# Kernel optimization log

Hardware: AMD Instinct MI355X
Metric: run time of the kernel (lower is better)

Reference implementation:

```python
import jax, jax.numpy as jnp
import numpy as np

C_HID = 128   # c = int(c2 * e) = 128
N_EXP = 4
TOP_K = 2


def conv2d(x, w, b, padding='SAME'):
    # x: [B,Cin,H,W], w: [Cout,Cin,kh,kw]
    out = jax.lax.conv_general_dilated(
        x, w, window_strides=(1, 1), padding=padding,
        dimension_numbers=('NCHW', 'OIHW', 'NCHW'))
    return out + b[None, :, None, None]


def silu(x):
    return x * jax.nn.sigmoid(x)


def setup_inputs() -> dict:
    key = jax.random.key(0)
    ks = jax.random.split(key, 10)
    B, C1, H, W = 16, 256, 80, 80
    c = C_HID
    s = 0.05
    return {
        'x': jax.random.normal(ks[0], (B, C1, H, W), jnp.float32),
        'W_cv1': jax.random.normal(ks[1], (2 * c, C1, 1, 1), jnp.float32) * s,
        'b_cv1': jax.random.normal(ks[2], (2 * c,), jnp.float32) * s,
        'W_r': jax.random.normal(ks[3], (N_EXP, c), jnp.float32) * s,
        'b_r': jax.random.normal(ks[4], (N_EXP,), jnp.float32) * s,
        'W_exp': jax.random.normal(ks[5], (N_EXP, c, c, 3, 3), jnp.float32) * s,
        'b_exp': jax.random.normal(ks[6], (N_EXP, c), jnp.float32) * s,
        'W_cv2': jax.random.normal(ks[7], (256, 3 * c, 1, 1), jnp.float32) * s,
        'b_cv2': jax.random.normal(ks[8], (256,), jnp.float32) * s,
    }


def reference(x, W_cv1, b_cv1, W_r, b_r, W_exp, b_exp, W_cv2, b_cv2):
    c = C_HID
    B = x.shape[0]
    # cv1: 1x1 conv -> SiLU (BN folded into bias), split into two branches
    y = silu(conv2d(x, W_cv1, b_cv1))           # [B, 2c, H, W]
    a, m = y[:, :c], y[:, c:]                   # each [B, c, H, W]

    # CrossModalRouter: GAP -> linear -> softmax -> top-k -> renormalize
    pooled = m.mean(axis=(2, 3))                # [B, c]
    logits = pooled @ W_r.T + b_r               # [B, E]
    probs = jax.nn.softmax(logits, axis=-1)
    w, idx = jax.lax.top_k(probs, TOP_K)        # [B, k]
    w = w / w.sum(axis=-1, keepdims=True)

    # dense sparse-gate: zeros except the top-k entries
    gate = jnp.zeros((B, N_EXP), x.dtype).at[jnp.arange(B)[:, None], idx].set(w)

    # DualModalExpertContainer: E independent 3x3 conv+SiLU experts, gated sum
    exp_out = jax.vmap(lambda we, be: silu(conv2d(m, we, be)))(W_exp, b_exp)  # [E,B,c,H,W]
    moe = jnp.einsum('be,ebchw->bchw', gate, exp_out)  # [B, c, H, W]

    # cv2 over concat([y0, y1, expert_out])
    out = silu(conv2d(jnp.concatenate([a, m, moe], axis=1), W_cv2, b_cv2))
    return out
```

## Files before the change

### kernel.cpp

```cpp
#include <hip/hip_runtime.h>
#include <hip/hip_bf16.h>

#define NPIX 6400
#define IMW 80
#define IMH 80

typedef __attribute__((ext_vector_type(8))) short short8;
typedef __attribute__((ext_vector_type(4))) float floatx4;

__device__ __forceinline__ float silu_f(float v) {
    return v / (1.0f + __expf(-v));
}
__device__ __forceinline__ unsigned short f2bf(float v) {
    __hip_bfloat16 h = __float2bfloat16(v);
    return *(unsigned short*)&h;
}


__global__ __launch_bounds__(256) void prep_swz1(
    const float* __restrict__ W1, __hip_bfloat16* __restrict__ Wt1s)
{
    int t = blockIdx.x * 256 + threadIdx.x;
    int mt = t >> 9, rem = t & 511;
    int ks = rem >> 6, lane = rem & 63;
    int col = lane & 15, quad = lane >> 4;
    const float* src = W1 + (size_t)(mt * 16 + col) * 256 + ks * 32 + quad * 8;
    unsigned short pk[8];
    #pragma unroll
    for (int j = 0; j < 8; ++j) pk[j] = f2bf(src[j]);
    *(uint4*)(Wt1s + (size_t)t * 8) = *(uint4*)pk;
}

__global__ __launch_bounds__(256) void prep_swz2(
    const float* __restrict__ W2, __hip_bfloat16* __restrict__ Wt2s)
{
    int t = blockIdx.x * 256 + threadIdx.x;
    int mt = t / 768, rem = t % 768;
    int ks = rem >> 6, lane = rem & 63;
    int col = lane & 15, quad = lane >> 4;
    const float* src = W2 + (size_t)(mt * 16 + col) * 384 + ks * 32 + quad * 8;
    unsigned short pk[8];
    #pragma unroll
    for (int j = 0; j < 8; ++j) pk[j] = f2bf(src[j]);
    *(uint4*)(Wt2s + (size_t)t * 8) = *(uint4*)pk;
}

__global__ __launch_bounds__(256) void prep_swzE(
    const float* __restrict__ Wexp, __hip_bfloat16* __restrict__ Wts)
{
    int t = blockIdx.x * 256 + threadIdx.x;
    int e = t / 18432, rem = t % 18432;
    int gmt = rem / 2304, rem2 = rem % 2304;
    int s = rem2 >> 6, lane = rem2 & 63;
    int col = lane & 15, quad = lane >> 4;
    int tap = s >> 2;
    int cib = (s & 3) * 32 + quad * 8;
    int co  = gmt * 16 + col;
    const float* src = Wexp + ((size_t)(e * 128 + co) * 128 + cib) * 9 + tap;
    unsigned short pk[8];
    #pragma unroll
    for (int j = 0; j < 8; ++j) pk[j] = f2bf(src[j * 9]);
    *(uint4*)(Wts + (size_t)t * 8) = *(uint4*)pk;
}

__global__ __launch_bounds__(256) void transpose_x(
    const float* __restrict__ x, __hip_bfloat16* __restrict__ catT)
{
    const int b   = blockIdx.z;
    const int ci0 = blockIdx.y * 64;
    const int p0  = blockIdx.x * 64;
    __shared__ unsigned short t[64][70];
    const int tid = threadIdx.x;
    const float* src = x + ((size_t)b * 256 + ci0) * NPIX + p0;
    #pragma unroll
    for (int it = 0; it < 4; ++it) {
        int idx = tid + it * 256;
        int ci = idx >> 4, pg = idx & 15;
        float4 v = *(const float4*)(src + (size_t)ci * NPIX + pg * 4);
        t[pg * 4 + 0][ci] = f2bf(v.x);
        t[pg * 4 + 1][ci] = f2bf(v.y);
        t[pg * 4 + 2][ci] = f2bf(v.z);
        t[pg * 4 + 3][ci] = f2bf(v.w);
    }
    __syncthreads();
    unsigned short* dst = (unsigned short*)catT + ((size_t)b * NPIX + p0) * 384 + ci0;
    #pragma unroll
    for (int it = 0; it < 2; ++it) {
        int idx = tid + it * 256;
        int p = idx >> 3, cg = idx & 7;
        unsigned short vv[8];
        #pragma unroll
        for (int j = 0; j < 8; ++j) vv[j] = t[p][cg * 8 + j];
        *(uint4*)(dst + (size_t)p * 384 + cg * 8) = *(uint4*)vv;
    }
}

__global__ __launch_bounds__(256, 2) void cv1_mfma(
    const __hip_bfloat16* __restrict__ Wt1s, const float* __restrict__ b1,
    __hip_bfloat16* __restrict__ catT, float* __restrict__ pooled)
{
    const int b  = blockIdx.y;
    const int p0 = blockIdx.x * 128;
    const int tid = threadIdx.x;
    const int wave = tid >> 6, lane = tid & 63;
    const int col = lane & 15, quad = lane >> 4;
    const int cohalf  = (wave & 1) * 128;
    const int gmt0    = (wave & 1) * 8;
    const int pixhalf = (wave >> 1) * 64;

    __hip_bfloat16* ct = catT + (size_t)b * NPIX * 384;
    int pp[4];
    #pragma unroll
    for (int nt = 0; nt < 4; ++nt) pp[nt] = p0 + pixhalf + nt * 16 + col;

    floatx4 acc[8][4] = {};

    #pragma unroll
    for (int ks = 0; ks < 8; ++ks) {
        short8 bf[4];
        #pragma unroll
        for (int nt = 0; nt < 4; ++nt)
            bf[nt] = *(const short8*)&ct[(size_t)pp[nt] * 384 + ks * 32 + quad * 8];
        #pragma unroll
        for (int mt = 0; mt < 8; ++mt) {
            short8 af = *(const short8*)&Wt1s[(size_t)(((gmt0 + mt) * 8 + ks) * 64 + lane) * 8];
            #pragma unroll
            for (int nt = 0; nt < 4; ++nt)
                acc[mt][nt] = __builtin_amdgcn_mfma_f32_16x16x32_bf16(af, bf[nt], acc[mt][nt], 0, 0, 0);
        }
    }

    __syncthreads();

    #pragma unroll
    for (int mt = 0; mt < 8; ++mt) {
        const int cobase = cohalf + mt * 16 + quad * 4;
        float bias[4];
        #pragma unroll
        for (int r = 0; r < 4; ++r) bias[r] = b1[cobase + r];
        float v[4][4];
        #pragma unroll
        for (int nt = 0; nt < 4; ++nt) {
            unsigned short pk[4];
            #pragma unroll
            for (int r = 0; r < 4; ++r) {
                v[nt][r] = silu_f(acc[mt][nt][r] + bias[r]);
                pk[r] = f2bf(v[nt][r]);
            }
            *(uint2*)&ct[(size_t)pp[nt] * 384 + cobase] = *(uint2*)pk;
        }
        if (cohalf == 128) {
            #pragma unroll
            for (int r = 0; r < 4; ++r) {
                float s = v[0][r] + v[1][r] + v[2][r] + v[3][r];
                #pragma unroll
                for (int m = 1; m < 16; m <<= 1)
                    s += __shfl_xor(s, m, 64);
                if (col == 0)
                    atomicAdd(&pooled[b * 128 + (cobase - 128) + r], s * (1.0f / NPIX));
            }
        }
    }
}

__global__ __launch_bounds__(64) void router_kernel(
    const float* __restrict__ pooled, const float* __restrict__ Wr,
    const float* __restrict__ br, int* __restrict__ sel_idx, float* __restrict__ sel_w)
{
    __shared__ float lg[16][4];
    int tid = threadIdx.x;
    int b = tid >> 2, e = tid & 3;
    float s = br[e];
    for (int c2 = 0; c2 < 128; c2++)
        s += pooled[b * 128 + c2] * Wr[e * 128 + c2];
    lg[b][e] = s;
    __syncthreads();
    if (tid < 16) {
        int bb = tid;
        float l[4]; float mx = -1e30f;
        #pragma unroll
        for (int i = 0; i < 4; i++) { l[i] = lg[bb][i]; mx = fmaxf(mx, l[i]); }
        float p[4]; float sum = 0.f;
        #pragma unroll
        for (int i = 0; i < 4; i++) { p[i] = __expf(l[i] - mx); sum += p[i]; }
        #pragma unroll
        for (int i = 0; i < 4; i++) p[i] /= sum;
        int i1 = 0;
        for (int i = 1; i < 4; i++) if (p[i] > p[i1]) i1 = i;
        int i2 = (i1 == 0) ? 1 : 0;
        for (int i = 0; i < 4; i++) if (i != i1 && p[i] > p[i2]) i2 = i;
        float inv = 1.0f / (p[i1] + p[i2]);
        sel_idx[bb * 2 + 0] = i1; sel_idx[bb * 2 + 1] = i2;
        sel_w[bb * 2 + 0] = p[i1] * inv; sel_w[bb * 2 + 1] = p[i2] * inv;
    }
}

__global__ __launch_bounds__(256, 2) void expert_gemm(
    __hip_bfloat16* __restrict__ catT, const __hip_bfloat16* __restrict__ Wts,
    const float* __restrict__ bexp, const int* __restrict__ sel_idx,
    const float* __restrict__ sel_w)
{
    const int id  = blockIdx.x;
    const int xcd = id & 7, j = id >> 3;
    const int lin = xcd * 100 + j;
    const int b   = lin / 50;
    const int p0  = (lin % 50) * 128;

    const int e0 = sel_idx[b * 2 + 0], e1 = sel_idx[b * 2 + 1];
    const float g0 = sel_w[b * 2 + 0], g1 = sel_w[b * 2 + 1];

    const int tid  = threadIdx.x;
    const int wave = tid >> 6, lane = tid & 63;
    const int col  = lane & 15, quad = lane >> 4;
    const int cohalf  = (wave & 1) * 64;
    const int gmt0    = (wave & 1) * 4;
    const int pixhalf = (wave >> 1) * 64;

    __hip_bfloat16* ct = catT + (size_t)b * NPIX * 384;
    const __hip_bfloat16* wsrc[2];
    wsrc[0] = Wts + (size_t)e0 * (8 * 36 * 64 * 8) + (size_t)lane * 8;
    wsrc[1] = Wts + (size_t)e1 * (8 * 36 * 64 * 8) + (size_t)lane * 8;

    int pp[4], prow[4], pcol[4];
    #pragma unroll
    for (int nt = 0; nt < 4; ++nt) {
        pp[nt]   = p0 + pixhalf + nt * 16 + col;
        prow[nt] = pp[nt] / IMW;
        pcol[nt] = pp[nt] % IMW;
    }

    floatx4 acc[2][4][4] = {};

    for (int tap = 0; tap < 9; ++tap) {
        const int dyy = tap / 3 - 1, dxx = tap % 3 - 1;
        bool valid[4];
        const __hip_bfloat16* bbase[4];
        #pragma unroll
        for (int nt = 0; nt < 4; ++nt) {
            int ir = prow[nt] + dyy, ic = pcol[nt] + dxx;
            valid[nt] = ((unsigned)ir < IMH) && ((unsigned)ic < IMW);
            bbase[nt] = ct + (size_t)(ir * IMW + ic) * 384 + 128 + quad * 8;
        }
        #pragma unroll
        for (int ss = 0; ss < 4; ++ss) {
            const int s = tap * 4 + ss;
            short8 bf[4];
            #pragma unroll
            for (int nt = 0; nt < 4; ++nt) {
                int4 vv = {0, 0, 0, 0};
                if (valid[nt]) vv = *(const int4*)(bbase[nt] + ss * 32);
                bf[nt] = *(short8*)&vv;
            }
            __builtin_amdgcn_s_setprio(1);
            #pragma unroll
            for (int e = 0; e < 2; ++e) {
                #pragma unroll
                for (int mt = 0; mt < 4; ++mt) {
                    short8 af = *(const short8*)(wsrc[e]
                                 + (size_t)((gmt0 + mt) * 36 + s) * 64 * 8);
                    #pragma unroll
                    for (int nt = 0; nt < 4; ++nt)
                        acc[e][mt][nt] = __builtin_amdgcn_mfma_f32_16x16x32_bf16(
                            af, bf[nt], acc[e][mt][nt], 0, 0, 0);
                }
            }
            __builtin_amdgcn_s_setprio(0);
        }
    }

    #pragma unroll
    for (int mt = 0; mt < 4; ++mt) {
        const int cobase = cohalf + mt * 16 + quad * 4;
        #pragma unroll
        for (int nt = 0; nt < 4; ++nt) {
            unsigned short pk[4];
            #pragma unroll
            for (int r = 0; r < 4; ++r) {
                int coo = cobase + r;
                float vb0 = bexp[e0 * 128 + coo];
                float vb1 = bexp[e1 * 128 + coo];
                float v = g0 * silu_f(acc[0][mt][nt][r] + vb0)
                        + g1 * silu_f(acc[1][mt][nt][r] + vb1);
                pk[r] = f2bf(v);
            }
            *(uint2*)&ct[(size_t)pp[nt] * 384 + 256 + cobase] = *(uint2*)pk;
        }
    }
}

__global__ __launch_bounds__(256, 2) void cv2_mfma(
    const __hip_bfloat16* __restrict__ catT, const __hip_bfloat16* __restrict__ Wt2s,
    const float* __restrict__ b2, float* __restrict__ out)
{
    const int b  = blockIdx.y;
    const int p0 = blockIdx.x * 128;
    const int tid = threadIdx.x;
    const int wave = tid >> 6, lane = tid & 63;
    const int col = lane & 15, quad = lane >> 4;
    const int cohalf  = (wave & 1) * 128;
    const int gmt0    = (wave & 1) * 8;
    const int pixhalf = (wave >> 1) * 64;

    const __hip_bfloat16* ct = catT + (size_t)b * NPIX * 384;
    int pp[4];
    #pragma unroll
    for (int nt = 0; nt < 4; ++nt) pp[nt] = p0 + pixhalf + nt * 16 + col;

    floatx4 acc[8][4] = {};

    #pragma unroll
    for (int ks = 0; ks < 12; ++ks) {
        short8 bf[4];
        #pragma unroll
        for (int nt = 0; nt < 4; ++nt)
            bf[nt] = *(const short8*)&ct[(size_t)pp[nt] * 384 + ks * 32 + quad * 8];
        #pragma unroll
        for (int mt = 0; mt < 8; ++mt) {
            short8 af = *(const short8*)&Wt2s[(size_t)(((gmt0 + mt) * 12 + ks) * 64 + lane) * 8];
            #pragma unroll
            for (int nt = 0; nt < 4; ++nt)
                acc[mt][nt] = __builtin_amdgcn_mfma_f32_16x16x32_bf16(af, bf[nt], acc[mt][nt], 0, 0, 0);
        }
    }

    #pragma unroll
    for (int mt = 0; mt < 8; ++mt) {
        const int cobase = cohalf + mt * 16 + quad * 4;
        #pragma unroll
        for (int r = 0; r < 4; ++r) {
            float bias = b2[cobase + r];
            size_t rowb = ((size_t)b * 256 + cobase + r) * NPIX;
            #pragma unroll
            for (int nt = 0; nt < 4; ++nt)
                out[rowb + pp[nt]] = silu_f(acc[mt][nt][r] + bias);
        }
    }
}

extern "C" void kernel_launch(void* const* d_in, const int* in_sizes, int n_in,
                              void* d_out, int out_size, void* d_ws, size_t ws_size,
                              hipStream_t stream)
{
    (void)in_sizes; (void)n_in; (void)out_size; (void)ws_size;
    const float* x    = (const float*)d_in[0];
    const float* W1   = (const float*)d_in[1];
    const float* b1   = (const float*)d_in[2];
    const float* Wr   = (const float*)d_in[3];
    const float* br   = (const float*)d_in[4];
    const float* Wexp = (const float*)d_in[5];
    const float* bexp = (const float*)d_in[6];
    const float* W2   = (const float*)d_in[7];
    const float* b2   = (const float*)d_in[8];
    float* out = (float*)d_out;

    char* ws = (char*)d_ws;
    __hip_bfloat16* catT = (__hip_bfloat16*)ws;
    __hip_bfloat16* Wts  = (__hip_bfloat16*)(ws + 78643200);
    __hip_bfloat16* Wt1s = (__hip_bfloat16*)(ws + 79822848);
    __hip_bfloat16* Wt2s = (__hip_bfloat16*)(ws + 79953920);
    float* pooled        = (float*)(ws + 80150528);
    int*   sel_idx       = (int*)(ws + 80158720);
    float* sel_w         = (float*)(ws + 80158848);

    hipMemsetAsync(pooled, 0, 16 * 128 * 4, stream);
    prep_swz1    <<<dim3(32),         256, 0, stream>>>(W1, Wt1s);
    prep_swz2    <<<dim3(48),         256, 0, stream>>>(W2, Wt2s);
    prep_swzE    <<<dim3(288),        256, 0, stream>>>(Wexp, Wts);
    transpose_x  <<<dim3(100, 4, 16), 256, 0, stream>>>(x, catT);
    cv1_mfma     <<<dim3(50, 16),     256, 0, stream>>>(Wt1s, b1, catT, pooled);
    router_kernel<<<1,                 64, 0, stream>>>(pooled, Wr, br, sel_idx, sel_w);
    expert_gemm  <<<dim3(800),        256, 0, stream>>>(catT, Wts, bexp, sel_idx, sel_w);
    cv2_mfma     <<<dim3(50, 16),     256, 0, stream>>>(catT, Wt2s, b2, out);
}
```

Baseline: 469.5 us.

## Fuse input transpose and bf16 conversion into cv1 MFMA kernel via LDS

Removes the separate transpose_x kernel. cv1 now loads the fp32 input tile directly, converts it to bf16 and stores it in a 64KB XOR-swizzled shared buffer, then feeds the MFMA B operands from LDS instead of catT in global memory. This removes one kernel launch and the write and re-read of the x part of catT. In exchange it uses 64KB of LDS per block, which may limit occupancy to below the declared two blocks per CU. The per-thread load loop also strides across channels, which may coalesce poorly.

After: 452.2 us. -3.7%, faster.

```diff
diff --git a/kernel.cpp b/kernel.cpp
--- a/kernel.cpp
+++ b/kernel.cpp
@@ -63,45 +63,35 @@
     *(uint4*)(Wts + (size_t)t * 8) = *(uint4*)pk;
 }
 
-__global__ __launch_bounds__(256) void transpose_x(
-    const float* __restrict__ x, __hip_bfloat16* __restrict__ catT)
-{
-    const int b   = blockIdx.z;
-    const int ci0 = blockIdx.y * 64;
-    const int p0  = blockIdx.x * 64;
-    __shared__ unsigned short t[64][70];
-    const int tid = threadIdx.x;
-    const float* src = x + ((size_t)b * 256 + ci0) * NPIX + p0;
-    #pragma unroll
-    for (int it = 0; it < 4; ++it) {
-        int idx = tid + it * 256;
-        int ci = idx >> 4, pg = idx & 15;
-        float4 v = *(const float4*)(src + (size_t)ci * NPIX + pg * 4);
-        t[pg * 4 + 0][ci] = f2bf(v.x);
-        t[pg * 4 + 1][ci] = f2bf(v.y);
-        t[pg * 4 + 2][ci] = f2bf(v.z);
-        t[pg * 4 + 3][ci] = f2bf(v.w);
-    }
-    __syncthreads();
-    unsigned short* dst = (unsigned short*)catT + ((size_t)b * NPIX + p0) * 384 + ci0;
-    #pragma unroll
-    for (int it = 0; it < 2; ++it) {
-        int idx = tid + it * 256;
-        int p = idx >> 3, cg = idx & 7;
-        unsigned short vv[8];
-        #pragma unroll
-        for (int j = 0; j < 8; ++j) vv[j] = t[p][cg * 8 + j];
-        *(uint4*)(dst + (size_t)p * 384 + cg * 8) = *(uint4*)vv;
-    }
-}
-
-__global__ __launch_bounds__(256, 2) void cv1_mfma(
-    const __hip_bfloat16* __restrict__ Wt1s, const float* __restrict__ b1,
-    __hip_bfloat16* __restrict__ catT, float* __restrict__ pooled)
-{
+__global__ __launch_bounds__(256, 2) void cv1_fused(
+    const float* __restrict__ x, const __hip_bfloat16* __restrict__ Wt1s,
+    const float* __restrict__ b1, __hip_bfloat16* __restrict__ catT,
+    float* __restrict__ pooled)
+{
+    __shared__ __align__(16) unsigned short xs[128][256];
     const int b  = blockIdx.y;
     const int p0 = blockIdx.x * 128;
     const int tid = threadIdx.x;
+
+    {
+        const int ci = tid;
+        const int slotbase = (ci >> 3) ;
+        const int cilo = ci & 7;
+        const float* src = x + ((size_t)b * 256 + ci) * NPIX + p0;
+        #pragma unroll
+        for (int pg = 0; pg < 32; ++pg) {
+            float4 v = *(const float4*)(src + pg * 4);
+            float vv[4] = {v.x, v.y, v.z, v.w};
+            #pragma unroll
+            for (int r = 0; r < 4; ++r) {
+                int pix = pg * 4 + r;
+                int slot = slotbase ^ ((pix & 7) << 2);
+                xs[pix][slot * 8 + cilo] = f2bf(vv[r]);
+            }
+        }
+    }
+    __syncthreads();
+
     const int wave = tid >> 6, lane = tid & 63;
     const int col = lane & 15, quad = lane >> 4;
     const int cohalf  = (wave & 1) * 128;
@@ -109,9 +99,12 @@
     const int pixhalf = (wave >> 1) * 64;
 
     __hip_bfloat16* ct = catT + (size_t)b * NPIX * 384;
-    int pp[4];
-    #pragma unroll
-    for (int nt = 0; nt < 4; ++nt) pp[nt] = p0 + pixhalf + nt * 16 + col;
+    int pp[4], pl[4];
+    #pragma unroll
+    for (int nt = 0; nt < 4; ++nt) {
+        pl[nt] = pixhalf + nt * 16 + col;
+        pp[nt] = p0 + pl[nt];
+    }
 
     floatx4 acc[8][4] = {};
 
@@ -119,8 +112,10 @@
     for (int ks = 0; ks < 8; ++ks) {
         short8 bf[4];
         #pragma unroll
-        for (int nt = 0; nt < 4; ++nt)
-            bf[nt] = *(const short8*)&ct[(size_t)pp[nt] * 384 + ks * 32 + quad * 8];
+        for (int nt = 0; nt < 4; ++nt) {
+            int slot = (ks * 4 + quad) ^ ((pl[nt] & 7) << 2);
+            bf[nt] = *(const short8*)&xs[pl[nt]][slot * 8];
+        }
         #pragma unroll
         for (int mt = 0; mt < 8; ++mt) {
             short8 af = *(const short8*)&Wt1s[(size_t)(((gmt0 + mt) * 8 + ks) * 64 + lane) * 8];
@@ -129,8 +124,6 @@
                 acc[mt][nt] = __builtin_amdgcn_mfma_f32_16x16x32_bf16(af, bf[nt], acc[mt][nt], 0, 0, 0);
         }
     }
-
-    __syncthreads();
 
     #pragma unroll
     for (int mt = 0; mt < 8; ++mt) {
@@ -366,8 +359,7 @@
     prep_swz1    <<<dim3(32),         256, 0, stream>>>(W1, Wt1s);
     prep_swz2    <<<dim3(48),         256, 0, stream>>>(W2, Wt2s);
     prep_swzE    <<<dim3(288),        256, 0, stream>>>(Wexp, Wts);
-    transpose_x  <<<dim3(100, 4, 16), 256, 0, stream>>>(x, catT);
-    cv1_mfma     <<<dim3(50, 16),     256, 0, stream>>>(Wt1s, b1, catT, pooled);
+    cv1_fused    <<<dim3(50, 16),     256, 0, stream>>>(x, Wt1s, b1, catT, pooled);
     router_kernel<<<1,                 64, 0, stream>>>(pooled, Wr, br, sel_idx, sel_w);
     expert_gemm  <<<dim3(800),        256, 0, stream>>>(catT, Wts, bexp, sel_idx, sel_w);
     cv2_mfma     <<<dim3(50, 16),     256, 0, stream>>>(catT, Wt2s, b2, out);
```
